# Kernel optimization log

Measured on AMD Instinct MI355X. Metric: run time of the kernel, lower is better.

Reference implementation:

```python
import jax, jax.numpy as jnp
import numpy as np

B, T_ENC, T_OUT = 64, 1024, 1000
N_MELS, ENC_D, DEC_H, ATTN_D = 80, 256, 256, 256


def setup_inputs() -> dict:
    key = jax.random.key(0)
    ks = jax.random.split(key, 24)

    def p(k, shape, scale=0.05):
        return jax.random.normal(k, shape, dtype=jnp.float32) * scale

    lengths = jax.random.randint(ks[0], (B,), T_ENC // 2, T_ENC + 1)
    enc_mask = (jnp.arange(T_ENC)[None, :] < lengths[:, None]).astype(jnp.float32)
    return {
        "enc_outputs": jax.random.normal(ks[1], (B, T_ENC, ENC_D), dtype=jnp.float32),
        "target_mel": jax.random.normal(ks[2], (B, T_OUT, N_MELS), dtype=jnp.float32),
        # attention params
        "W_enc": p(ks[3], (ATTN_D, ENC_D)), "b_enc": jnp.zeros((ATTN_D,), jnp.float32),
        "W_dec": p(ks[4], (ATTN_D, DEC_H)), "b_dec": jnp.zeros((ATTN_D,), jnp.float32),
        "v_w": p(ks[5], (1, ATTN_D)), "v_b": jnp.zeros((1,), jnp.float32),
        # prenet
        "pre_W1": p(ks[6], (DEC_H, N_MELS)), "pre_b1": jnp.zeros((DEC_H,), jnp.float32),
        "pre_W2": p(ks[7], (DEC_H, DEC_H)), "pre_b2": jnp.zeros((DEC_H,), jnp.float32),
        # LSTMCell (PyTorch gate order i, f, g, o)
        "W_ih": p(ks[8], (4 * DEC_H, DEC_H + ENC_D)), "W_hh": p(ks[9], (4 * DEC_H, DEC_H)),
        "b_ih": jnp.zeros((4 * DEC_H,), jnp.float32), "b_hh": jnp.zeros((4 * DEC_H,), jnp.float32),
        # output heads
        "mel_W": p(ks[10], (N_MELS, DEC_H + ENC_D)), "mel_b": jnp.zeros((N_MELS,), jnp.float32),
        "stop_W": p(ks[11], (1, DEC_H + ENC_D)), "stop_b": jnp.zeros((1,), jnp.float32),
        "enc_mask": enc_mask,
    }


def reference(enc_outputs, target_mel, W_enc, b_enc, W_dec, b_dec, v_w, v_b,
              pre_W1, pre_b1, pre_W2, pre_b2, W_ih, W_hh, b_ih, b_hh,
              mel_W, mel_b, stop_W, stop_b, enc_mask):
    Bsz = enc_outputs.shape[0]
    H = W_hh.shape[1]
    NEG = jnp.float32(-1e9)
    # precompute encoder projection once, as the original does
    attn_enc = jnp.einsum('bte,ae->bta', enc_outputs, W_enc) + b_enc  # (B, T_enc, A)
    # teacher forcing: input at step t is target_mel[t-1], zeros at t=0
    prev_inputs = jnp.concatenate(
        [jnp.zeros_like(target_mel[:, :1]), target_mel[:, :-1]], axis=1)
    xs = jnp.swapaxes(prev_inputs, 0, 1)  # (T_out, B, n_mels)

    def step(carry, prev):
        h, c = carry
        attn_dec = h @ W_dec.T + b_dec                                  # (B, A)
        energy = jnp.tanh(attn_enc + attn_dec[:, None, :]) @ v_w[0] + v_b[0]  # (B, T_enc)
        energy = jnp.where(enc_mask == 0, NEG, energy)
        attn = jax.nn.softmax(energy, axis=-1)
        context = jnp.einsum('bt,btd->bd', attn, enc_outputs)           # (B, enc_d)
        pre = jax.nn.relu(prev @ pre_W1.T + pre_b1)                     # dropout = identity (eval)
        pre = jax.nn.relu(pre @ pre_W2.T + pre_b2)
        x = jnp.concatenate([pre, context], axis=1)
        gates = x @ W_ih.T + b_ih + h @ W_hh.T + b_hh                   # (B, 4H)
        i, f, g, o = jnp.split(gates, 4, axis=1)
        c_new = jax.nn.sigmoid(f) * c + jax.nn.sigmoid(i) * jnp.tanh(g)
        h_new = jax.nn.sigmoid(o) * jnp.tanh(c_new)
        comb = jnp.concatenate([h_new, context], axis=1)
        mel = comb @ mel_W.T + mel_b
        stop = (comb @ stop_W.T + stop_b)[:, 0]
        return (h_new, c_new), (mel, stop)

    h0 = jnp.zeros((Bsz, H), dtype=enc_outputs.dtype)
    _, (mels, stops) = jax.lax.scan(step, (h0, h0), xs)
    return jnp.swapaxes(mels, 0, 1), jnp.swapaxes(stops, 0, 1)
```

## Files before the change

### kernel.cpp

```cpp
#include <hip/hip_runtime.h>
#include <hip/hip_bf16.h>

#define NMEL 80

typedef unsigned u32x4 __attribute__((ext_vector_type(4)));

__device__ __forceinline__ float bf2f(unsigned short u) {
  unsigned v = ((unsigned)u) << 16; float f; __builtin_memcpy(&f, &v, 4); return f;
}
__device__ __forceinline__ unsigned short f2bf_u(float f) {
  __hip_bfloat16 h = __float2bfloat16(f); unsigned short u; __builtin_memcpy(&u, &h, 2); return u;
}
__device__ __forceinline__ void unpk(unsigned u, float& lo, float& hi) {
  unsigned l = u << 16, h = u & 0xffff0000u;
  __builtin_memcpy(&lo, &l, 4); __builtin_memcpy(&hi, &h, 4);
}

constexpr size_t OFF_ATTNR = 0;
constexpr size_t SZ_ATTNR = (size_t)64 * 1024 * 256 * 2;
constexpr size_t OFF_ENCP = OFF_ATTNR + SZ_ATTNR;
constexpr size_t SZ_ENCP = (size_t)64 * 1024 * 256 * 2;
constexpr size_t OFF_PRE2 = OFF_ENCP + SZ_ENCP;
constexpr size_t SZ_PRE2 = (size_t)64000 * 256 * 2;
constexpr size_t OFF_WDT = OFF_PRE2 + SZ_PRE2;
constexpr size_t SZ_WDT = (size_t)65536 * 4;
constexpr size_t OFF_WHT = OFF_WDT + SZ_WDT;
constexpr size_t SZ_W1M = (size_t)262144 * 4;
constexpr size_t OFF_WCT = OFF_WHT + SZ_W1M;
constexpr size_t OFF_WPT = OFF_WCT + SZ_W1M;
constexpr size_t OFF_BIASG = OFF_WPT + SZ_W1M;
constexpr size_t SZ_BIASG = 1024 * 4;
constexpr size_t WS_NEED = OFF_BIASG + SZ_BIASG;

__global__ __launch_bounds__(256) void conv_encP(const float* __restrict__ enc,
                                                 u32x4* __restrict__ encP) {
  int idx = blockIdx.x * 256 + threadIdx.x;
  int b = idx >> 15, r = idx & 32767;
  int d8 = r >> 10, te = r & 1023;
  const float4* src = (const float4*)(enc + ((size_t)(b * 1024 + te)) * 256 + d8 * 8);
  float4 x0 = src[0], x1 = src[1];
  u32x4 o;
  o.x = (unsigned)f2bf_u(x0.x) | ((unsigned)f2bf_u(x0.y) << 16);
  o.y = (unsigned)f2bf_u(x0.z) | ((unsigned)f2bf_u(x0.w) << 16);
  o.z = (unsigned)f2bf_u(x1.x) | ((unsigned)f2bf_u(x1.y) << 16);
  o.w = (unsigned)f2bf_u(x1.z) | ((unsigned)f2bf_u(x1.w) << 16);
  encP[((size_t)(b * 32 + d8)) * 1024 + te] = o;
}

__global__ __launch_bounds__(256) void prep_w2(
    const float* __restrict__ W_dec, const float* __restrict__ W_hh,
    const float* __restrict__ W_ih, const float* __restrict__ b_ih,
    const float* __restrict__ b_hh,
    float* __restrict__ WdT, float* __restrict__ WhT,
    float* __restrict__ WcT, float* __restrict__ WpT, float* __restrict__ biasG) {
  int idx = blockIdx.x * 256 + threadIdx.x;
  if (idx < 65536) {
    int q = idx & 3, a = (idx >> 2) & 255, kq = idx >> 10;
    WdT[idx] = W_dec[(size_t)a * 256 + kq * 4 + q];
  } else if (idx < 327680) {
    int i = idx - 65536;
    int q = i & 3, g = (i >> 2) & 1023, kq = i >> 12;
    WhT[i] = W_hh[(size_t)g * 256 + kq * 4 + q];
  } else if (idx < 589824) {
    int i = idx - 327680;
    int q = i & 3, g = (i >> 2) & 1023, kq = i >> 12;
    WcT[i] = W_ih[(size_t)g * 512 + 256 + kq * 4 + q];
  } else if (idx < 851968) {
    int i = idx - 589824;
    int q = i & 3, g = (i >> 2) & 1023, kq = i >> 12;
    WpT[i] = W_ih[(size_t)g * 512 + kq * 4 + q];
  } else if (idx < 852992) {
    int g = idx - 851968;
    biasG[g] = b_ih[g] + b_hh[g];
  }
}

__global__ __launch_bounds__(256) void attn_gemm(const float* __restrict__ enc,
                                                 const float* __restrict__ W_enc,
                                                 const float* __restrict__ b_enc,
                                                 unsigned* __restrict__ attnR) {
  __shared__ unsigned short Alds[64 * 260];
  const int tid = threadIdx.x;
  const int row0 = blockIdx.x * 64;
  const int wv = tid >> 6, lane = tid & 63, nb = wv * 64;
  for (int idx = tid; idx < 64 * 256; idx += 256) {
    int r = idx >> 8, k = idx & 255;
    Alds[r * 260 + k] = f2bf_u(enc[(size_t)(row0 + r) * 256 + k]);
  }
  __syncthreads();
  float acc[64];
#pragma unroll
  for (int n = 0; n < 64; ++n) acc[n] = b_enc[nb + n];
  for (int k8 = 0; k8 < 256; k8 += 8) {
    ushort4 ua = *(const ushort4*)&Alds[lane * 260 + k8];
    ushort4 ub = *(const ushort4*)&Alds[lane * 260 + k8 + 4];
    float a0 = bf2f(ua.x), a1 = bf2f(ua.y), a2 = bf2f(ua.z), a3 = bf2f(ua.w);
    float a4 = bf2f(ub.x), a5 = bf2f(ub.y), a6 = bf2f(ub.z), a7 = bf2f(ub.w);
#pragma unroll
    for (int n = 0; n < 64; ++n) {
      const float4* wp = (const float4*)(W_enc + (size_t)(nb + n) * 256 + k8);
      float4 w0 = wp[0], w1 = wp[1];
      acc[n] = fmaf(a0, w0.x, acc[n]); acc[n] = fmaf(a1, w0.y, acc[n]);
      acc[n] = fmaf(a2, w0.z, acc[n]); acc[n] = fmaf(a3, w0.w, acc[n]);
      acc[n] = fmaf(a4, w1.x, acc[n]); acc[n] = fmaf(a5, w1.y, acc[n]);
      acc[n] = fmaf(a6, w1.z, acc[n]); acc[n] = fmaf(a7, w1.w, acc[n]);
    }
  }
  const float CE = 2.8853900817779268f;
  const int b = row0 >> 10;
  const int te_g = (row0 & 1023) + lane;
  const int sl = te_g >> 8, te_loc = te_g & 255;
#pragma unroll
  for (int n = 0; n < 64; n += 2) {
    int a = nb + n;
    unsigned pair = (unsigned)f2bf_u(acc[n] * CE) | ((unsigned)f2bf_u(acc[n + 1] * CE) << 16);
    size_t u4 = ((((size_t)(b * 4 + sl) * 4 + (a >> 6)) * 8 + ((a >> 3) & 7)) * 256 + te_loc);
    attnR[u4 * 4 + ((a & 7) >> 1)] = pair;
  }
}

__global__ __launch_bounds__(256) void prenet_fused(const float* __restrict__ tmel,
                                                    const float* __restrict__ W1,
                                                    const float* __restrict__ b1,
                                                    const float* __restrict__ W2,
                                                    const float* __restrict__ b2,
                                                    unsigned short* __restrict__ pre2) {
  __shared__ unsigned short Alds[64 * 260];
  const int tid = threadIdx.x;
  const int row0 = blockIdx.x * 64;
  const int wv = tid >> 6, lane = tid & 63, nb = wv * 64;
  for (int idx = tid; idx < 64 * 80; idx += 256) {
    int r = idx / 80, k = idx - r * 80;
    int R = row0 + r;
    float v = (R % 1000 != 0) ? tmel[(size_t)(R - 1) * NMEL + k] : 0.f;
    Alds[r * 260 + k] = f2bf_u(v);
  }
  __syncthreads();
  float acc[64];
#pragma unroll
  for (int n = 0; n < 64; ++n) acc[n] = b1[nb + n];
  for (int k8 = 0; k8 < 80; k8 += 8) {
    ushort4 ua = *(const ushort4*)&Alds[lane * 260 + k8];
    ushort4 ub = *(const ushort4*)&Alds[lane * 260 + k8 + 4];
    float a0 = bf2f(ua.x), a1 = bf2f(ua.y), a2 = bf2f(ua.z), a3 = bf2f(ua.w);
    float a4 = bf2f(ub.x), a5 = bf2f(ub.y), a6 = bf2f(ub.z), a7 = bf2f(ub.w);
#pragma unroll
    for (int n = 0; n < 64; ++n) {
      const float4* wp = (const float4*)(W1 + (size_t)(nb + n) * 80 + k8);
      float4 w0 = wp[0], w1 = wp[1];
      acc[n] = fmaf(a0, w0.x, acc[n]); acc[n] = fmaf(a1, w0.y, acc[n]);
      acc[n] = fmaf(a2, w0.z, acc[n]); acc[n] = fmaf(a3, w0.w, acc[n]);
      acc[n] = fmaf(a4, w1.x, acc[n]); acc[n] = fmaf(a5, w1.y, acc[n]);
      acc[n] = fmaf(a6, w1.z, acc[n]); acc[n] = fmaf(a7, w1.w, acc[n]);
    }
  }
  __syncthreads();
#pragma unroll
  for (int n = 0; n < 64; ++n) Alds[lane * 260 + nb + n] = f2bf_u(fmaxf(acc[n], 0.f));
  __syncthreads();
#pragma unroll
  for (int n = 0; n < 64; ++n) acc[n] = b2[nb + n];
  for (int k8 = 0; k8 < 256; k8 += 8) {
    ushort4 ua = *(const ushort4*)&Alds[lane * 260 + k8];
    ushort4 ub = *(const ushort4*)&Alds[lane * 260 + k8 + 4];
    float a0 = bf2f(ua.x), a1 = bf2f(ua.y), a2 = bf2f(ua.z), a3 = bf2f(ua.w);
    float a4 = bf2f(ub.x), a5 = bf2f(ub.y), a6 = bf2f(ub.z), a7 = bf2f(ub.w);
#pragma unroll
    for (int n = 0; n < 64; ++n) {
      const float4* wp = (const float4*)(W2 + (size_t)(nb + n) * 256 + k8);
      float4 w0 = wp[0], w1 = wp[1];
      acc[n] = fmaf(a0, w0.x, acc[n]); acc[n] = fmaf(a1, w0.y, acc[n]);
      acc[n] = fmaf(a2, w0.z, acc[n]); acc[n] = fmaf(a3, w0.w, acc[n]);
      acc[n] = fmaf(a4, w1.x, acc[n]); acc[n] = fmaf(a5, w1.y, acc[n]);
      acc[n] = fmaf(a6, w1.z, acc[n]); acc[n] = fmaf(a7, w1.w, acc[n]);
    }
  }
  __syncthreads();
#pragma unroll
  for (int n = 0; n < 64; ++n) Alds[lane * 260 + nb + n] = f2bf_u(fmaxf(acc[n], 0.f));
  __syncthreads();
  for (int idx = tid; idx < 64 * 128; idx += 256) {
    int r = idx >> 7, k2 = (idx & 127) * 2;
    unsigned pair = (unsigned)Alds[r * 260 + k2] | ((unsigned)Alds[r * 260 + k2 + 1] << 16);
    *(unsigned*)(pre2 + (size_t)(row0 + r) * 256 + k2) = pair;
  }
}

__global__ __launch_bounds__(1024) void decoder_one(
    const u32x4* __restrict__ attnR, const u32x4* __restrict__ encP,
    const unsigned short* __restrict__ pre2,
    const float4* __restrict__ WdT, const float4* __restrict__ WhT,
    const float4* __restrict__ WcT, const float4* __restrict__ WpT,
    const float* __restrict__ biasG,
    const float* __restrict__ b_dec, const float* __restrict__ v_w,
    const float* __restrict__ v_b, const float* __restrict__ enc_mask,
    const float* __restrict__ mel_W, const float* __restrict__ mel_b,
    const float* __restrict__ stop_W, const float* __restrict__ stop_b,
    float* __restrict__ out) {
  __shared__ __align__(16) float scratchB[8448];
  __shared__ __align__(16) float p_lds[1024];
  __shared__ __align__(16) float gates_lds[1024];
  __shared__ __align__(16) float h_lds[256];
  __shared__ __align__(16) float ctx_lds[256];
  __shared__ __align__(16) float pre_lds[256];
  __shared__ __align__(16) float dec_lds[256];
  __shared__ __align__(16) float v2_lds[256];
  __shared__ float red_lds[16];

  const int tid = threadIdx.x;
  const int b = blockIdx.x;
  const int t8 = tid & 255, chunk = tid >> 8;
  const int lane = tid & 63, wid = tid >> 6;
  const int d8 = tid >> 5, tec = tid & 31;
  const float CE = 2.8853900817779268f;
  const float L2E = 1.4426950408889634f;

  if (tid < 256) {
    h_lds[tid] = 0.f;
    float v = v_w[tid];
    v2_lds[tid] = -2.f * v;
    for (int m = 32; m; m >>= 1) v += __shfl_xor(v, m);
    if (lane == 0) red_lds[wid] = v;
  }
  float c_reg = 0.f;
  const float maskv = enc_mask[b * 1024 + tid];
  const float bdec_r = (tid < 256) ? b_dec[tid] : 0.f;
  const float biasg_r = biasG[tid];
  const float melb_r = (tid < 640 && (tid & 7) == 0) ? mel_b[tid >> 3] : 0.f;
  float stopw[8];
  if (wid == 11) {
#pragma unroll
    for (int i = 0; i < 8; ++i) stopw[i] = stop_W[lane * 8 + i];
  }
  __syncthreads();
  const float Sv_vb = red_lds[0] + red_lds[1] + red_lds[2] + red_lds[3] + v_b[0];
  const float stopb0 = stop_b[0];

  const u32x4* aB = attnR + (size_t)b * 32768 + chunk * 2048 + t8;
  const u32x4* eB = encP + ((size_t)(b * 32 + d8)) * 1024 + tec;
  const float4* wdB = WdT + chunk * 16 * 256 + t8;
  const float4* whB = WhT + tid;
  const float4* wcB = WcT + tid;
  const float4* wpB = WpT + tid;
  const unsigned short* pre2_b = pre2 + (size_t)b * 256000;
  float* outm = out + (size_t)b * 80000;
  float* outs = out + (size_t)5120000 + b * 1000;

  auto heads = [&](int ith) {
    if (tid < 640) {
      const int m = tid >> 3, q = tid & 7;
      float acc = melb_r;
      const float4* wm = (const float4*)(mel_W + (size_t)m * 512 + q * 64);
      const float4* xp = (q < 4) ? (const float4*)&h_lds[q * 64]
                                 : (const float4*)&ctx_lds[(q - 4) * 64];
#pragma unroll
      for (int i = 0; i < 16; ++i) {
        float4 w = wm[i]; float4 x = xp[i];
        acc = fmaf(w.x, x.x, acc); acc = fmaf(w.y, x.y, acc);
        acc = fmaf(w.z, x.z, acc); acc = fmaf(w.w, x.w, acc);
      }
      acc += __shfl_xor(acc, 1); acc += __shfl_xor(acc, 2); acc += __shfl_xor(acc, 4);
      if (q == 0) outm[ith * 80 + m] = acc;
    } else if (wid == 11) {
      float acc = 0.f;
#pragma unroll
      for (int i = 0; i < 8; ++i) {
        int cc = lane * 8 + i;
        float x = (cc < 256) ? h_lds[cc] : ctx_lds[cc - 256];
        acc = fmaf(stopw[i], x, acc);
      }
      for (int m = 32; m; m >>= 1) acc += __shfl_xor(acc, m);
      if (lane == 0) outs[ith] = acc + stopb0;
    }
  };

  float gph = 0.f;

  for (int it = 0; it < 1000; ++it) {
    {
      float acc = 0.f;
#pragma unroll
      for (int i = 0; i < 16; ++i) {
        float4 w = wdB[(size_t)i << 8];
        float4 h4 = *(const float4*)&h_lds[chunk * 64 + i * 4];
        acc = fmaf(w.x, h4.x, acc); acc = fmaf(w.y, h4.y, acc);
        acc = fmaf(w.z, h4.z, acc); acc = fmaf(w.w, h4.w, acc);
      }
      scratchB[(chunk << 8) + t8] = acc;
      if (tid < 256) pre_lds[tid] = bf2f(pre2_b[it * 256 + tid]);
      if (it > 0) heads(it - 1);
    }
    __syncthreads();
    if (tid < 256)
      dec_lds[tid] = (bdec_r + scratchB[tid] + scratchB[256 + tid] +
                      scratchB[512 + tid] + scratchB[768 + tid]) * CE;
    __syncthreads();
#pragma unroll 1
    for (int sl = 0; sl < 4; ++sl) {
      float acc = 0.f;
#pragma unroll
      for (int j = 0; j < 8; ++j) {
        u32x4 u = aB[sl * 8192 + j * 256];
        int ab = (chunk << 6) + (j << 3);
        float4 d0 = *(const float4*)&dec_lds[ab];
        float4 d1 = *(const float4*)&dec_lds[ab + 4];
        float4 v0 = *(const float4*)&v2_lds[ab];
        float4 v1 = *(const float4*)&v2_lds[ab + 4];
        float t0, t1, t2, t3, t4, t5, t6, t7;
        unpk(u.x, t0, t1); unpk(u.y, t2, t3); unpk(u.z, t4, t5); unpk(u.w, t6, t7);
        acc = fmaf(v0.x, __builtin_amdgcn_rcpf(1.f + __builtin_amdgcn_exp2f(t0 + d0.x)), acc);
        acc = fmaf(v0.y, __builtin_amdgcn_rcpf(1.f + __builtin_amdgcn_exp2f(t1 + d0.y)), acc);
        acc = fmaf(v0.z, __builtin_amdgcn_rcpf(1.f + __builtin_amdgcn_exp2f(t2 + d0.z)), acc);
        acc = fmaf(v0.w, __builtin_amdgcn_rcpf(1.f + __builtin_amdgcn_exp2f(t3 + d0.w)), acc);
        acc = fmaf(v1.x, __builtin_amdgcn_rcpf(1.f + __builtin_amdgcn_exp2f(t4 + d1.x)), acc);
        acc = fmaf(v1.y, __builtin_amdgcn_rcpf(1.f + __builtin_amdgcn_exp2f(t5 + d1.y)), acc);
        acc = fmaf(v1.z, __builtin_amdgcn_rcpf(1.f + __builtin_amdgcn_exp2f(t6 + d1.z)), acc);
        acc = fmaf(v1.w, __builtin_amdgcn_rcpf(1.f + __builtin_amdgcn_exp2f(t7 + d1.w)), acc);
      }
      scratchB[sl * 1024 + (chunk << 8) + t8] = acc;
    }
    __syncthreads();
    {
      int base = (tid >> 8) * 1024 + (tid & 255);
      float e = Sv_vb + scratchB[base] + scratchB[base + 256] +
                scratchB[base + 512] + scratchB[base + 768];
      float p = (maskv != 0.f) ? __builtin_amdgcn_exp2f(e * L2E) : 0.f;
      p_lds[tid] = p;
      for (int m = 32; m; m >>= 1) p += __shfl_xor(p, m);
      if (lane == 0) red_lds[wid] = p;
    }
    __syncthreads();
    {
      gph = biasg_r;
      float cc0 = 0, cc1 = 0, cc2 = 0, cc3 = 0, cc4 = 0, cc5 = 0, cc6 = 0, cc7 = 0;
      u32x4 eb[8];
      auto issueQ = [&](int q0) {
#pragma unroll
        for (int t = 0; t < 8; ++t)
          eb[t] = eB[((q0 << 3) + t) << 5];
      };
      auto consumeQ = [&](int q0) {
#pragma unroll
        for (int t = 0; t < 8; ++t) {
          float pv = p_lds[((((q0 << 3) + t) << 5)) + tec];
          float e0, e1, e2, e3, e4, e5, e6, e7;
          unpk(eb[t].x, e0, e1); unpk(eb[t].y, e2, e3);
          unpk(eb[t].z, e4, e5); unpk(eb[t].w, e6, e7);
          cc0 = fmaf(pv, e0, cc0); cc1 = fmaf(pv, e1, cc1);
          cc2 = fmaf(pv, e2, cc2); cc3 = fmaf(pv, e3, cc3);
          cc4 = fmaf(pv, e4, cc4); cc5 = fmaf(pv, e5, cc5);
          cc6 = fmaf(pv, e6, cc6); cc7 = fmaf(pv, e7, cc7);
        }
      };
      auto gdot = [&](const float4* __restrict__ wB, const float* __restrict__ xl, int i0) {
#pragma unroll 8
        for (int i = i0; i < i0 + 32; ++i) {
          float4 w = wB[(size_t)i << 10];
          float4 x = *(const float4*)&xl[i << 2];
          gph = fmaf(w.x, x.x, gph); gph = fmaf(w.y, x.y, gph);
          gph = fmaf(w.z, x.z, gph); gph = fmaf(w.w, x.w, gph);
        }
      };
      issueQ(0); gdot(wpB, pre_lds, 0);  consumeQ(0);
      issueQ(1); gdot(wpB, pre_lds, 32); consumeQ(1);
      issueQ(2); gdot(whB, h_lds, 0);    consumeQ(2);
      issueQ(3); gdot(whB, h_lds, 32);   consumeQ(3);
      float* cb = &scratchB[(d8 << 3) * 33 + tec];
      cb[0] = cc0; cb[33] = cc1; cb[66] = cc2; cb[99] = cc3;
      cb[132] = cc4; cb[165] = cc5; cb[198] = cc6; cb[231] = cc7;
    }
    __syncthreads();
    if (tid < 256) {
      float S = red_lds[0] + red_lds[1] + red_lds[2] + red_lds[3] +
                red_lds[4] + red_lds[5] + red_lds[6] + red_lds[7] +
                red_lds[8] + red_lds[9] + red_lds[10] + red_lds[11] +
                red_lds[12] + red_lds[13] + red_lds[14] + red_lds[15];
      float rS = 1.f / S;
      float s = 0.f;
      const float* row = &scratchB[tid * 33];
#pragma unroll
      for (int t = 0; t < 32; ++t) s += row[t];
      ctx_lds[tid] = s * rS;
    }
    __syncthreads();
    {
      float g = gph;
#pragma unroll 8
      for (int i = 0; i < 64; ++i) {
        float4 w = wcB[(size_t)i << 10];
        float4 x = *(const float4*)&ctx_lds[i << 2];
        g = fmaf(w.x, x.x, g); g = fmaf(w.y, x.y, g);
        g = fmaf(w.z, x.z, g); g = fmaf(w.w, x.w, g);
      }
      gates_lds[tid] = g;
    }
    __syncthreads();
    if (tid < 256) {
      float ii = gates_lds[tid], ff = gates_lds[256 + tid];
      float gg = gates_lds[512 + tid], oo = gates_lds[768 + tid];
      float si = __builtin_amdgcn_rcpf(1.f + __builtin_amdgcn_exp2f(-ii * L2E));
      float sf = __builtin_amdgcn_rcpf(1.f + __builtin_amdgcn_exp2f(-ff * L2E));
      float so = __builtin_amdgcn_rcpf(1.f + __builtin_amdgcn_exp2f(-oo * L2E));
      float tg2 = 1.f - 2.f * __builtin_amdgcn_rcpf(1.f + __builtin_amdgcn_exp2f(gg * CE));
      float cn = sf * c_reg + si * tg2;
      float tc = 1.f - 2.f * __builtin_amdgcn_rcpf(1.f + __builtin_amdgcn_exp2f(cn * CE));
      c_reg = cn;
      h_lds[tid] = so * tc;
    }
    __syncthreads();
  }
  heads(999);
}

extern "C" void kernel_launch(void* const* d_in, const int* in_sizes, int n_in,
                              void* d_out, int out_size, void* d_ws, size_t ws_size,
                              hipStream_t stream) {
  const float* enc = (const float*)d_in[0];
  const float* tmel = (const float*)d_in[1];
  const float* W_enc = (const float*)d_in[2];
  const float* b_enc = (const float*)d_in[3];
  const float* W_dec = (const float*)d_in[4];
  const float* b_dec = (const float*)d_in[5];
  const float* v_w = (const float*)d_in[6];
  const float* v_b = (const float*)d_in[7];
  const float* pW1 = (const float*)d_in[8];
  const float* pb1 = (const float*)d_in[9];
  const float* pW2 = (const float*)d_in[10];
  const float* pb2 = (const float*)d_in[11];
  const float* W_ih = (const float*)d_in[12];
  const float* W_hh = (const float*)d_in[13];
  const float* b_ih = (const float*)d_in[14];
  const float* b_hh = (const float*)d_in[15];
  const float* mel_W = (const float*)d_in[16];
  const float* mel_b = (const float*)d_in[17];
  const float* stop_W = (const float*)d_in[18];
  const float* stop_b = (const float*)d_in[19];
  const float* emask = (const float*)d_in[20];

  if (ws_size < WS_NEED) return;

  char* ws = (char*)d_ws;
  unsigned* attnR = (unsigned*)(ws + OFF_ATTNR);
  u32x4* encP = (u32x4*)(ws + OFF_ENCP);
  unsigned short* pre2 = (unsigned short*)(ws + OFF_PRE2);
  float* WdT = (float*)(ws + OFF_WDT);
  float* WhT = (float*)(ws + OFF_WHT);
  float* WcT = (float*)(ws + OFF_WCT);
  float* WpT = (float*)(ws + OFF_WPT);
  float* biasG = (float*)(ws + OFF_BIASG);

  conv_encP<<<8192, 256, 0, stream>>>(enc, encP);
  prep_w2<<<3332, 256, 0, stream>>>(W_dec, W_hh, W_ih, b_ih, b_hh, WdT, WhT, WcT, WpT, biasG);
  attn_gemm<<<1024, 256, 0, stream>>>(enc, W_enc, b_enc, attnR);
  prenet_fused<<<1000, 256, 0, stream>>>(tmel, pW1, pb1, pW2, pb2, pre2);
  decoder_one<<<64, 1024, 0, stream>>>(
      (const u32x4*)attnR, (const u32x4*)encP, pre2,
      (const float4*)WdT, (const float4*)WhT, (const float4*)WcT, (const float4*)WpT,
      biasG, b_dec, v_w, v_b, emask, mel_W, mel_b, stop_W, stop_b, (float*)d_out);
}
```

Before: 172.1 ms.

## Split each batch decoder across 8 workgroups with global-memory barrier exchange

The single 1024-thread workgroup per batch element is replaced by 8 cooperating 256-thread workgroups per batch (512 total). Each one owns 128 encoder timesteps, keeps its slice of the attention projection in LDS and its encoder slice in registers, and computes one eighth of the gate rows. Partial context sums, softmax denominators and gate values are exchanged through global memory using atomic counters and spin-wait barriers, twice per timestep. This spreads the serial recurrence over many more compute units and drops the separate encoder-repacking kernel. In exchange it adds cross-workgroup synchronisation latency every step, and it relies on all 512 workgroups being co-resident, so it could deadlock if they are not.

```diff
diff --git a/kernel.cpp b/kernel.cpp
--- a/kernel.cpp
+++ b/kernel.cpp
@@ -15,12 +15,16 @@
   unsigned l = u << 16, h = u & 0xffff0000u;
   __builtin_memcpy(&lo, &l, 4); __builtin_memcpy(&hi, &h, 4);
 }
-
-constexpr size_t OFF_ATTNR = 0;
-constexpr size_t SZ_ATTNR = (size_t)64 * 1024 * 256 * 2;
-constexpr size_t OFF_ENCP = OFF_ATTNR + SZ_ATTNR;
-constexpr size_t SZ_ENCP = (size_t)64 * 1024 * 256 * 2;
-constexpr size_t OFF_PRE2 = OFF_ENCP + SZ_ENCP;
+__device__ __forceinline__ float agload(const float* p) {
+  return __hip_atomic_load(p, __ATOMIC_RELAXED, __HIP_MEMORY_SCOPE_AGENT);
+}
+__device__ __forceinline__ void agstore(float* p, float v) {
+  __hip_atomic_store(p, v, __ATOMIC_RELAXED, __HIP_MEMORY_SCOPE_AGENT);
+}
+
+constexpr size_t OFF_ATTNT = 0;
+constexpr size_t SZ_ATTNT = (size_t)65536 * 256 * 2;
+constexpr size_t OFF_PRE2 = OFF_ATTNT + SZ_ATTNT;
 constexpr size_t SZ_PRE2 = (size_t)64000 * 256 * 2;
 constexpr size_t OFF_WDT = OFF_PRE2 + SZ_PRE2;
 constexpr size_t SZ_WDT = (size_t)65536 * 4;
@@ -30,22 +34,13 @@
 constexpr size_t OFF_WPT = OFF_WCT + SZ_W1M;
 constexpr size_t OFF_BIASG = OFF_WPT + SZ_W1M;
 constexpr size_t SZ_BIASG = 1024 * 4;
-constexpr size_t WS_NEED = OFF_BIASG + SZ_BIASG;
-
-__global__ __launch_bounds__(256) void conv_encP(const float* __restrict__ enc,
-                                                 u32x4* __restrict__ encP) {
-  int idx = blockIdx.x * 256 + threadIdx.x;
-  int b = idx >> 15, r = idx & 32767;
-  int d8 = r >> 10, te = r & 1023;
-  const float4* src = (const float4*)(enc + ((size_t)(b * 1024 + te)) * 256 + d8 * 8);
-  float4 x0 = src[0], x1 = src[1];
-  u32x4 o;
-  o.x = (unsigned)f2bf_u(x0.x) | ((unsigned)f2bf_u(x0.y) << 16);
-  o.y = (unsigned)f2bf_u(x0.z) | ((unsigned)f2bf_u(x0.w) << 16);
-  o.z = (unsigned)f2bf_u(x1.x) | ((unsigned)f2bf_u(x1.y) << 16);
-  o.w = (unsigned)f2bf_u(x1.z) | ((unsigned)f2bf_u(x1.w) << 16);
-  encP[((size_t)(b * 32 + d8)) * 1024 + te] = o;
-}
+constexpr size_t OFF_EXCH = (OFF_BIASG + SZ_BIASG + 255) & ~(size_t)255;
+constexpr size_t EXF_CTX = 0;
+constexpr size_t EXF_S = EXF_CTX + (size_t)512 * 256;
+constexpr size_t EXF_G = EXF_S + 512;
+constexpr size_t EXF_CTR = EXF_G + (size_t)512 * 128;
+constexpr size_t EXCH_FLOATS = EXF_CTR + 64;
+constexpr size_t WS_NEED = OFF_EXCH + EXCH_FLOATS * 4;
 
 __global__ __launch_bounds__(256) void prep_w2(
     const float* __restrict__ W_dec, const float* __restrict__ W_hh,
@@ -78,7 +73,7 @@
 __global__ __launch_bounds__(256) void attn_gemm(const float* __restrict__ enc,
                                                  const float* __restrict__ W_enc,
                                                  const float* __restrict__ b_enc,
-                                                 unsigned* __restrict__ attnR) {
+                                                 unsigned* __restrict__ attnT) {
   __shared__ unsigned short Alds[64 * 260];
   const int tid = threadIdx.x;
   const int row0 = blockIdx.x * 64;
@@ -107,16 +102,10 @@
     }
   }
   const float CE = 2.8853900817779268f;
-  const int b = row0 >> 10;
-  const int te_g = (row0 & 1023) + lane;
-  const int sl = te_g >> 8, te_loc = te_g & 255;
-#pragma unroll
-  for (int n = 0; n < 64; n += 2) {
-    int a = nb + n;
-    unsigned pair = (unsigned)f2bf_u(acc[n] * CE) | ((unsigned)f2bf_u(acc[n + 1] * CE) << 16);
-    size_t u4 = ((((size_t)(b * 4 + sl) * 4 + (a >> 6)) * 8 + ((a >> 3) & 7)) * 256 + te_loc);
-    attnR[u4 * 4 + ((a & 7) >> 1)] = pair;
-  }
+  unsigned* rowp = attnT + (size_t)(row0 + lane) * 128 + (nb >> 1);
+#pragma unroll
+  for (int n = 0; n < 64; n += 2)
+    rowp[n >> 1] = (unsigned)f2bf_u(acc[n] * CE) | ((unsigned)f2bf_u(acc[n + 1] * CE) << 16);
 }
 
 __global__ __launch_bounds__(256) void prenet_fused(const float* __restrict__ tmel,
@@ -186,49 +175,49 @@
   }
 }
 
-__global__ __launch_bounds__(1024) void decoder_one(
-    const u32x4* __restrict__ attnR, const u32x4* __restrict__ encP,
+__global__ __launch_bounds__(256, 2) void decoder_split(
+    const unsigned* __restrict__ attnT, const float* __restrict__ enc,
     const unsigned short* __restrict__ pre2,
-    const float4* __restrict__ WdT, const float4* __restrict__ WhT,
+    const float* __restrict__ WdT, const float4* __restrict__ WhT,
     const float4* __restrict__ WcT, const float4* __restrict__ WpT,
     const float* __restrict__ biasG,
     const float* __restrict__ b_dec, const float* __restrict__ v_w,
     const float* __restrict__ v_b, const float* __restrict__ enc_mask,
     const float* __restrict__ mel_W, const float* __restrict__ mel_b,
     const float* __restrict__ stop_W, const float* __restrict__ stop_b,
-    float* __restrict__ out) {
-  __shared__ __align__(16) float scratchB[8448];
-  __shared__ __align__(16) float p_lds[1024];
-  __shared__ __align__(16) float gates_lds[1024];
+    float* exch, unsigned* ctr, float* __restrict__ out) {
+  __shared__ __align__(16) unsigned short attn_lds[128 * 260];
+  __shared__ __align__(16) float dec_lds[256];
+  __shared__ __align__(16) float v2_lds[256];
   __shared__ __align__(16) float h_lds[256];
   __shared__ __align__(16) float ctx_lds[256];
   __shared__ __align__(16) float pre_lds[256];
-  __shared__ __align__(16) float dec_lds[256];
-  __shared__ __align__(16) float v2_lds[256];
+  __shared__ __align__(16) float ctxp_lds[4 * 256];
+  __shared__ __align__(16) float scratch[256];
+  __shared__ float p_lds[128];
   __shared__ float red_lds[16];
 
   const int tid = threadIdx.x;
-  const int b = blockIdx.x;
-  const int t8 = tid & 255, chunk = tid >> 8;
-  const int lane = tid & 63, wid = tid >> 6;
-  const int d8 = tid >> 5, tec = tid & 31;
+  const int b = blockIdx.x >> 3, s = blockIdx.x & 7;
+  const int tloc = tid & 127, chunk = tid >> 7;
+  const int lane = tid & 63, w = tid >> 6;
   const float CE = 2.8853900817779268f;
   const float L2E = 1.4426950408889634f;
 
-  if (tid < 256) {
-    h_lds[tid] = 0.f;
+  h_lds[tid] = 0.f;
+  {
     float v = v_w[tid];
     v2_lds[tid] = -2.f * v;
     for (int m = 32; m; m >>= 1) v += __shfl_xor(v, m);
-    if (lane == 0) red_lds[wid] = v;
+    if (lane == 0) red_lds[w] = v;
   }
   float c_reg = 0.f;
-  const float maskv = enc_mask[b * 1024 + tid];
-  const float bdec_r = (tid < 256) ? b_dec[tid] : 0.f;
-  const float biasg_r = biasG[tid];
-  const float melb_r = (tid < 640 && (tid & 7) == 0) ? mel_b[tid >> 3] : 0.f;
+  const float maskv = (tid < 128) ? enc_mask[b * 1024 + s * 128 + tloc] : 0.f;
+  const float bdec_r = b_dec[tid];
+  const float biasg_r = biasG[s * 128 + tloc];
+  const float melb_r = (tid < 160 && (tid & 1) == 0) ? mel_b[tid >> 1] : 0.f;
   float stopw[8];
-  if (wid == 11) {
+  if (w == 3) {
 #pragma unroll
     for (int i = 0; i < 8; ++i) stopw[i] = stop_W[lane * 8 + i];
   }
@@ -236,168 +225,166 @@
   const float Sv_vb = red_lds[0] + red_lds[1] + red_lds[2] + red_lds[3] + v_b[0];
   const float stopb0 = stop_b[0];
 
-  const u32x4* aB = attnR + (size_t)b * 32768 + chunk * 2048 + t8;
-  const u32x4* eB = encP + ((size_t)(b * 32 + d8)) * 1024 + tec;
-  const float4* wdB = WdT + chunk * 16 * 256 + t8;
-  const float4* whB = WhT + tid;
-  const float4* wcB = WcT + tid;
-  const float4* wpB = WpT + tid;
+  {
+    const unsigned* aT = attnT + ((size_t)(b * 1024 + s * 128)) * 128;
+    for (int idx = tid; idx < 128 * 128; idx += 256) {
+      int r = idx >> 7, c2 = idx & 127;
+      *(unsigned*)&attn_lds[r * 260 + c2 * 2] = aT[(size_t)r * 128 + c2];
+    }
+  }
+  uint2 enc_r2[32];
+  {
+    const float4* eF = (const float4*)enc + ((size_t)(b * 1024 + s * 128 + w * 32)) * 64 + lane;
+#pragma unroll
+    for (int i = 0; i < 32; ++i) {
+      float4 x = eF[(size_t)i << 6];
+      enc_r2[i].x = (unsigned)f2bf_u(x.x) | ((unsigned)f2bf_u(x.y) << 16);
+      enc_r2[i].y = (unsigned)f2bf_u(x.z) | ((unsigned)f2bf_u(x.w) << 16);
+    }
+#pragma unroll
+    for (int i = 0; i < 32; ++i) { asm volatile("" : "+v"(enc_r2[i].x)); asm volatile("" : "+v"(enc_r2[i].y)); }
+  }
+  __syncthreads();
+
+  float* ctxP = exch + EXF_CTX;
+  float* sP = exch + EXF_S;
+  float* gP = exch + EXF_G;
+  unsigned* ctrb = ctr + b;
+  unsigned epoch = 0;
+
+  const float4* wd = (const float4*)WdT + tid;
+  const float4* wpB = WpT + (s * 128 + tloc);
+  const float4* wcB = WcT + (s * 128 + tloc);
+  const float4* whB = WhT + (s * 128 + tloc);
   const unsigned short* pre2_b = pre2 + (size_t)b * 256000;
   float* outm = out + (size_t)b * 80000;
   float* outs = out + (size_t)5120000 + b * 1000;
 
-  auto heads = [&](int ith) {
-    if (tid < 640) {
-      const int m = tid >> 3, q = tid & 7;
-      float acc = melb_r;
-      const float4* wm = (const float4*)(mel_W + (size_t)m * 512 + q * 64);
-      const float4* xp = (q < 4) ? (const float4*)&h_lds[q * 64]
-                                 : (const float4*)&ctx_lds[(q - 4) * 64];
-#pragma unroll
-      for (int i = 0; i < 16; ++i) {
-        float4 w = wm[i]; float4 x = xp[i];
-        acc = fmaf(w.x, x.x, acc); acc = fmaf(w.y, x.y, acc);
-        acc = fmaf(w.z, x.z, acc); acc = fmaf(w.w, x.w, acc);
-      }
-      acc += __shfl_xor(acc, 1); acc += __shfl_xor(acc, 2); acc += __shfl_xor(acc, 4);
-      if (q == 0) outm[ith * 80 + m] = acc;
-    } else if (wid == 11) {
-      float acc = 0.f;
-#pragma unroll
-      for (int i = 0; i < 8; ++i) {
-        int cc = lane * 8 + i;
-        float x = (cc < 256) ? h_lds[cc] : ctx_lds[cc - 256];
-        acc = fmaf(stopw[i], x, acc);
-      }
-      for (int m = 32; m; m >>= 1) acc += __shfl_xor(acc, m);
-      if (lane == 0) outs[ith] = acc + stopb0;
-    }
-  };
-
-  float gph = 0.f;
-
   for (int it = 0; it < 1000; ++it) {
     {
-      float acc = 0.f;
-#pragma unroll
-      for (int i = 0; i < 16; ++i) {
-        float4 w = wdB[(size_t)i << 8];
-        float4 h4 = *(const float4*)&h_lds[chunk * 64 + i * 4];
-        acc = fmaf(w.x, h4.x, acc); acc = fmaf(w.y, h4.y, acc);
-        acc = fmaf(w.z, h4.z, acc); acc = fmaf(w.w, h4.w, acc);
-      }
-      scratchB[(chunk << 8) + t8] = acc;
-      if (tid < 256) pre_lds[tid] = bf2f(pre2_b[it * 256 + tid]);
-      if (it > 0) heads(it - 1);
-    }
-    __syncthreads();
-    if (tid < 256)
-      dec_lds[tid] = (bdec_r + scratchB[tid] + scratchB[256 + tid] +
-                      scratchB[512 + tid] + scratchB[768 + tid]) * CE;
-    __syncthreads();
-#pragma unroll 1
-    for (int sl = 0; sl < 4; ++sl) {
-      float acc = 0.f;
-#pragma unroll
-      for (int j = 0; j < 8; ++j) {
-        u32x4 u = aB[sl * 8192 + j * 256];
-        int ab = (chunk << 6) + (j << 3);
-        float4 d0 = *(const float4*)&dec_lds[ab];
-        float4 d1 = *(const float4*)&dec_lds[ab + 4];
-        float4 v0 = *(const float4*)&v2_lds[ab];
-        float4 v1 = *(const float4*)&v2_lds[ab + 4];
-        float t0, t1, t2, t3, t4, t5, t6, t7;
-        unpk(u.x, t0, t1); unpk(u.y, t2, t3); unpk(u.z, t4, t5); unpk(u.w, t6, t7);
-        acc = fmaf(v0.x, __builtin_amdgcn_rcpf(1.f + __builtin_amdgcn_exp2f(t0 + d0.x)), acc);
-        acc = fmaf(v0.y, __builtin_amdgcn_rcpf(1.f + __builtin_amdgcn_exp2f(t1 + d0.y)), acc);
-        acc = fmaf(v0.z, __builtin_amdgcn_rcpf(1.f + __builtin_amdgcn_exp2f(t2 + d0.z)), acc);
-        acc = fmaf(v0.w, __builtin_amdgcn_rcpf(1.f + __builtin_amdgcn_exp2f(t3 + d0.w)), acc);
-        acc = fmaf(v1.x, __builtin_amdgcn_rcpf(1.f + __builtin_amdgcn_exp2f(t4 + d1.x)), acc);
-        acc = fmaf(v1.y, __builtin_amdgcn_rcpf(1.f + __builtin_amdgcn_exp2f(t5 + d1.y)), acc);
-        acc = fmaf(v1.z, __builtin_amdgcn_rcpf(1.f + __builtin_amdgcn_exp2f(t6 + d1.z)), acc);
-        acc = fmaf(v1.w, __builtin_amdgcn_rcpf(1.f + __builtin_amdgcn_exp2f(t7 + d1.w)), acc);
-      }
-      scratchB[sl * 1024 + (chunk << 8) + t8] = acc;
-    }
-    __syncthreads();
-    {
-      int base = (tid >> 8) * 1024 + (tid & 255);
-      float e = Sv_vb + scratchB[base] + scratchB[base + 256] +
-                scratchB[base + 512] + scratchB[base + 768];
+      pre_lds[tid] = bf2f(pre2_b[it * 256 + tid]);
+      float acc = bdec_r;
+#pragma unroll 8
+      for (int kq = 0; kq < 64; ++kq) {
+        float4 wv = wd[(size_t)kq << 8];
+        float4 h4 = *(const float4*)&h_lds[kq << 2];
+        acc = fmaf(wv.x, h4.x, acc); acc = fmaf(wv.y, h4.y, acc);
+        acc = fmaf(wv.z, h4.z, acc); acc = fmaf(wv.w, h4.w, acc);
+      }
+      dec_lds[tid] = acc * CE;
+    }
+    __syncthreads();
+    {
+      float eacc = 0.f;
+      const unsigned short* arow = &attn_lds[tloc * 260 + chunk * 128];
+#pragma unroll 8
+      for (int q = 0; q < 32; ++q) {
+        ushort4 ua = *(const ushort4*)&arow[q * 4];
+        int ab = chunk * 128 + q * 4;
+        float4 d = *(const float4*)&dec_lds[ab];
+        float4 v = *(const float4*)&v2_lds[ab];
+        eacc = fmaf(v.x, __builtin_amdgcn_rcpf(1.f + __builtin_amdgcn_exp2f(bf2f(ua.x) + d.x)), eacc);
+        eacc = fmaf(v.y, __builtin_amdgcn_rcpf(1.f + __builtin_amdgcn_exp2f(bf2f(ua.y) + d.y)), eacc);
+        eacc = fmaf(v.z, __builtin_amdgcn_rcpf(1.f + __builtin_amdgcn_exp2f(bf2f(ua.z) + d.z)), eacc);
+        eacc = fmaf(v.w, __builtin_amdgcn_rcpf(1.f + __builtin_amdgcn_exp2f(bf2f(ua.w) + d.w)), eacc);
+      }
+      scratch[chunk * 128 + tloc] = eacc;
+    }
+    __syncthreads();
+    if (tid < 128) {
+      float e = Sv_vb + scratch[tid] + scratch[128 + tid];
       float p = (maskv != 0.f) ? __builtin_amdgcn_exp2f(e * L2E) : 0.f;
       p_lds[tid] = p;
       for (int m = 32; m; m >>= 1) p += __shfl_xor(p, m);
-      if (lane == 0) red_lds[wid] = p;
-    }
-    __syncthreads();
-    {
-      gph = biasg_r;
-      float cc0 = 0, cc1 = 0, cc2 = 0, cc3 = 0, cc4 = 0, cc5 = 0, cc6 = 0, cc7 = 0;
-      u32x4 eb[8];
-      auto issueQ = [&](int q0) {
-#pragma unroll
-        for (int t = 0; t < 8; ++t)
-          eb[t] = eB[((q0 << 3) + t) << 5];
-      };
-      auto consumeQ = [&](int q0) {
-#pragma unroll
-        for (int t = 0; t < 8; ++t) {
-          float pv = p_lds[((((q0 << 3) + t) << 5)) + tec];
-          float e0, e1, e2, e3, e4, e5, e6, e7;
-          unpk(eb[t].x, e0, e1); unpk(eb[t].y, e2, e3);
-          unpk(eb[t].z, e4, e5); unpk(eb[t].w, e6, e7);
-          cc0 = fmaf(pv, e0, cc0); cc1 = fmaf(pv, e1, cc1);
-          cc2 = fmaf(pv, e2, cc2); cc3 = fmaf(pv, e3, cc3);
-          cc4 = fmaf(pv, e4, cc4); cc5 = fmaf(pv, e5, cc5);
-          cc6 = fmaf(pv, e6, cc6); cc7 = fmaf(pv, e7, cc7);
-        }
-      };
-      auto gdot = [&](const float4* __restrict__ wB, const float* __restrict__ xl, int i0) {
-#pragma unroll 8
-        for (int i = i0; i < i0 + 32; ++i) {
-          float4 w = wB[(size_t)i << 10];
-          float4 x = *(const float4*)&xl[i << 2];
-          gph = fmaf(w.x, x.x, gph); gph = fmaf(w.y, x.y, gph);
-          gph = fmaf(w.z, x.z, gph); gph = fmaf(w.w, x.w, gph);
-        }
-      };
-      issueQ(0); gdot(wpB, pre_lds, 0);  consumeQ(0);
-      issueQ(1); gdot(wpB, pre_lds, 32); consumeQ(1);
-      issueQ(2); gdot(whB, h_lds, 0);    consumeQ(2);
-      issueQ(3); gdot(whB, h_lds, 32);   consumeQ(3);
-      float* cb = &scratchB[(d8 << 3) * 33 + tec];
-      cb[0] = cc0; cb[33] = cc1; cb[66] = cc2; cb[99] = cc3;
-      cb[132] = cc4; cb[165] = cc5; cb[198] = cc6; cb[231] = cc7;
-    }
-    __syncthreads();
-    if (tid < 256) {
-      float S = red_lds[0] + red_lds[1] + red_lds[2] + red_lds[3] +
-                red_lds[4] + red_lds[5] + red_lds[6] + red_lds[7] +
-                red_lds[8] + red_lds[9] + red_lds[10] + red_lds[11] +
+      if (lane == 0) red_lds[w] = p;
+    }
+    __syncthreads();
+    {
+      float c0 = 0, c1 = 0, c2 = 0, c3 = 0;
+#pragma unroll
+      for (int i = 0; i < 32; ++i) {
+        float pv = p_lds[w * 32 + i];
+        float e0, e1, e2, e3;
+        unpk(enc_r2[i].x, e0, e1);
+        unpk(enc_r2[i].y, e2, e3);
+        c0 = fmaf(pv, e0, c0); c1 = fmaf(pv, e1, c1);
+        c2 = fmaf(pv, e2, c2); c3 = fmaf(pv, e3, c3);
+      }
+      float* cb = &ctxp_lds[w * 256 + lane * 4];
+      cb[0] = c0; cb[1] = c1; cb[2] = c2; cb[3] = c3;
+    }
+    __syncthreads();
+    {
+      float cp = ctxp_lds[tid] + ctxp_lds[256 + tid] + ctxp_lds[512 + tid] + ctxp_lds[768 + tid];
+      agstore(&ctxP[(size_t)(b * 8 + s) * 256 + tid], cp);
+    }
+    if (tid == 0) agstore(&sP[b * 8 + s], red_lds[0] + red_lds[1]);
+    __threadfence();
+    __syncthreads();
+    if (tid == 0) {
+      ++epoch;
+      __hip_atomic_fetch_add(ctrb, 1u, __ATOMIC_RELEASE, __HIP_MEMORY_SCOPE_AGENT);
+      while (__hip_atomic_load(ctrb, __ATOMIC_ACQUIRE, __HIP_MEMORY_SCOPE_AGENT) < 8u * epoch)
+        __builtin_amdgcn_s_sleep(1);
+    }
+    __syncthreads();
+    {
+      if (tid < 8) red_lds[8 + tid] = agload(&sP[b * 8 + tid]);
+      float csum = 0.f;
+#pragma unroll
+      for (int sp = 0; sp < 8; ++sp) csum += agload(&ctxP[(size_t)(b * 8 + sp) * 256 + tid]);
+      __syncthreads();
+      float S = red_lds[8] + red_lds[9] + red_lds[10] + red_lds[11] +
                 red_lds[12] + red_lds[13] + red_lds[14] + red_lds[15];
-      float rS = 1.f / S;
-      float s = 0.f;
-      const float* row = &scratchB[tid * 33];
-#pragma unroll
-      for (int t = 0; t < 32; ++t) s += row[t];
-      ctx_lds[tid] = s * rS;
-    }
-    __syncthreads();
-    {
-      float g = gph;
-#pragma unroll 8
-      for (int i = 0; i < 64; ++i) {
-        float4 w = wcB[(size_t)i << 10];
-        float4 x = *(const float4*)&ctx_lds[i << 2];
-        g = fmaf(w.x, x.x, g); g = fmaf(w.y, x.y, g);
-        g = fmaf(w.z, x.z, g); g = fmaf(w.w, x.w, g);
-      }
-      gates_lds[tid] = g;
-    }
-    __syncthreads();
-    if (tid < 256) {
-      float ii = gates_lds[tid], ff = gates_lds[256 + tid];
-      float gg = gates_lds[512 + tid], oo = gates_lds[768 + tid];
+      ctx_lds[tid] = csum * (1.f / S);
+    }
+    __syncthreads();
+    {
+      float gacc = 0.f;
+      const int k0 = chunk * 32;
+#pragma unroll 8
+      for (int kq = k0; kq < k0 + 32; ++kq) {
+        float4 wv = wpB[(size_t)kq << 10];
+        float4 x = *(const float4*)&pre_lds[kq << 2];
+        gacc = fmaf(wv.x, x.x, gacc); gacc = fmaf(wv.y, x.y, gacc);
+        gacc = fmaf(wv.z, x.z, gacc); gacc = fmaf(wv.w, x.w, gacc);
+      }
+#pragma unroll 8
+      for (int kq = k0; kq < k0 + 32; ++kq) {
+        float4 wv = wcB[(size_t)kq << 10];
+        float4 x = *(const float4*)&ctx_lds[kq << 2];
+        gacc = fmaf(wv.x, x.x, gacc); gacc = fmaf(wv.y, x.y, gacc);
+        gacc = fmaf(wv.z, x.z, gacc); gacc = fmaf(wv.w, x.w, gacc);
+      }
+#pragma unroll 8
+      for (int kq = k0; kq < k0 + 32; ++kq) {
+        float4 wv = whB[(size_t)kq << 10];
+        float4 x = *(const float4*)&h_lds[kq << 2];
+        gacc = fmaf(wv.x, x.x, gacc); gacc = fmaf(wv.y, x.y, gacc);
+        gacc = fmaf(wv.z, x.z, gacc); gacc = fmaf(wv.w, x.w, gacc);
+      }
+      scratch[chunk * 128 + tloc] = gacc;
+    }
+    __syncthreads();
+    if (tid < 128) {
+      float g = biasg_r + scratch[tid] + scratch[128 + tid];
+      agstore(&gP[(size_t)(b * 8 + s) * 128 + tid], g);
+    }
+    __threadfence();
+    __syncthreads();
+    if (tid == 0) {
+      ++epoch;
+      __hip_atomic_fetch_add(ctrb, 1u, __ATOMIC_RELEASE, __HIP_MEMORY_SCOPE_AGENT);
+      while (__hip_atomic_load(ctrb, __ATOMIC_ACQUIRE, __HIP_MEMORY_SCOPE_AGENT) < 8u * epoch)
+        __builtin_amdgcn_s_sleep(1);
+    }
+    __syncthreads();
+    {
+      const int hi = tid >> 7, lo = tid & 127;
+      float ii = agload(&gP[(size_t)(b * 8 + 0 + hi) * 128 + lo]);
+      float ff = agload(&gP[(size_t)(b * 8 + 2 + hi) * 128 + lo]);
+      float gg = agload(&gP[(size_t)(b * 8 + 4 + hi) * 128 + lo]);
+      float oo = agload(&gP[(size_t)(b * 8 + 6 + hi) * 128 + lo]);
       float si = __builtin_amdgcn_rcpf(1.f + __builtin_amdgcn_exp2f(-ii * L2E));
       float sf = __builtin_amdgcn_rcpf(1.f + __builtin_amdgcn_exp2f(-ff * L2E));
       float so = __builtin_amdgcn_rcpf(1.f + __builtin_amdgcn_exp2f(-oo * L2E));
@@ -408,8 +395,33 @@
       h_lds[tid] = so * tc;
     }
     __syncthreads();
-  }
-  heads(999);
+    if (s == 0) {
+      if (tid < 160) {
+        const int m = tid >> 1, q = tid & 1;
+        float acc2 = melb_r;
+        const float4* wm = (const float4*)(mel_W + (size_t)m * 512 + q * 256);
+        const float4* xp = (q == 0) ? (const float4*)h_lds : (const float4*)ctx_lds;
+#pragma unroll 8
+        for (int i = 0; i < 64; ++i) {
+          float4 wv = wm[i]; float4 x = xp[i];
+          acc2 = fmaf(wv.x, x.x, acc2); acc2 = fmaf(wv.y, x.y, acc2);
+          acc2 = fmaf(wv.z, x.z, acc2); acc2 = fmaf(wv.w, x.w, acc2);
+        }
+        acc2 += __shfl_xor(acc2, 1);
+        if (q == 0) outm[it * 80 + m] = acc2;
+      } else if (w == 3) {
+        float acc2 = 0.f;
+#pragma unroll
+        for (int i = 0; i < 8; ++i) {
+          int cc = lane * 8 + i;
+          float x = (cc < 256) ? h_lds[cc] : ctx_lds[cc - 256];
+          acc2 = fmaf(stopw[i], x, acc2);
+        }
+        for (int m = 32; m; m >>= 1) acc2 += __shfl_xor(acc2, m);
+        if (lane == 0) outs[it] = acc2 + stopb0;
+      }
+    }
+  }
 }
 
 extern "C" void kernel_launch(void* const* d_in, const int* in_sizes, int n_in,
@@ -440,21 +452,23 @@
   if (ws_size < WS_NEED) return;
 
   char* ws = (char*)d_ws;
-  unsigned* attnR = (unsigned*)(ws + OFF_ATTNR);
-  u32x4* encP = (u32x4*)(ws + OFF_ENCP);
+  unsigned* attnT = (unsigned*)(ws + OFF_ATTNT);
   unsigned short* pre2 = (unsigned short*)(ws + OFF_PRE2);
   float* WdT = (float*)(ws + OFF_WDT);
   float* WhT = (float*)(ws + OFF_WHT);
   float* WcT = (float*)(ws + OFF_WCT);
   float* WpT = (float*)(ws + OFF_WPT);
   float* biasG = (float*)(ws + OFF_BIASG);
-
-  conv_encP<<<8192, 256, 0, stream>>>(enc, encP);
+  float* exch = (float*)(ws + OFF_EXCH);
+  unsigned* ctr = (unsigned*)(exch + EXF_CTR);
+
+  hipMemsetAsync(exch, 0, EXCH_FLOATS * 4, stream);
+
   prep_w2<<<3332, 256, 0, stream>>>(W_dec, W_hh, W_ih, b_ih, b_hh, WdT, WhT, WcT, WpT, biasG);
-  attn_gemm<<<1024, 256, 0, stream>>>(enc, W_enc, b_enc, attnR);
+  attn_gemm<<<1024, 256, 0, stream>>>(enc, W_enc, b_enc, attnT);
   prenet_fused<<<1000, 256, 0, stream>>>(tmel, pW1, pb1, pW2, pb2, pre2);
-  decoder_one<<<64, 1024, 0, stream>>>(
-      (const u32x4*)attnR, (const u32x4*)encP, pre2,
-      (const float4*)WdT, (const float4*)WhT, (const float4*)WcT, (const float4*)WpT,
-      biasG, b_dec, v_w, v_b, emask, mel_W, mel_b, stop_W, stop_b, (float*)d_out);
-}
+  decoder_split<<<512, 256, 0, stream>>>(
+      attnT, enc, pre2, WdT, (const float4*)WhT, (const float4*)WcT, (const float4*)WpT,
+      biasG, b_dec, v_w, v_b, emask, mel_W, mel_b, stop_W, stop_b,
+      exch, ctr, (float*)d_out);
+}
```

Result: slower. 191.6 ms (+11.3%).
